# Optimization experiments

Hardware: AMD Instinct MI355X
Metric: run time of the kernel (lower is better)

The kernel has to match this reference:

```python
import jax, jax.numpy as jnp
import numpy as np
import math

NUM_HEADS = 16
HIDDEN = 1024
HEAD_DIM = HIDDEN // NUM_HEADS
MAX_POS = 512
BUCKET = 256
SCALE = 1.0 / math.sqrt(3.0 * HEAD_DIM)


def _make_log_bucket_position(rel_pos):
    # rel_pos: int32 [S, S]
    mid = BUCKET // 2
    rp = rel_pos.astype(jnp.float32)
    sign = jnp.sign(rp)
    abs_pos = jnp.where((rel_pos < mid) & (rel_pos > -mid), float(mid - 1), jnp.abs(rp))
    log_pos = jnp.ceil(jnp.log(abs_pos / mid) * (mid - 1) / math.log((MAX_POS - 1) / mid)) + mid
    bucket_pos = jnp.where(abs_pos <= mid, rp, log_pos * sign)
    return bucket_pos.astype(jnp.int32)


def _get_rel_pos(num_positions):
    ids = jnp.arange(num_positions, dtype=jnp.int32)
    rel_pos = ids[:, None] - ids[None, :]  # [S, S]
    return _make_log_bucket_position(rel_pos)


def setup_inputs() -> dict:
    key = jax.random.key(0)
    ks = jax.random.split(key, 10)
    B, S = 8, 512
    s_in = 1.0 / math.sqrt(HIDDEN)
    inputs = jax.random.normal(ks[0], (B, S, HIDDEN), dtype=jnp.float32)
    rel_embeddings = jax.random.normal(ks[1], (B, 2 * BUCKET, HIDDEN), dtype=jnp.float32)
    Wq = jax.random.normal(ks[2], (HIDDEN, NUM_HEADS, HEAD_DIM), dtype=jnp.float32) * s_in
    Wk = jax.random.normal(ks[3], (HIDDEN, NUM_HEADS, HEAD_DIM), dtype=jnp.float32) * s_in
    Wv = jax.random.normal(ks[4], (HIDDEN, NUM_HEADS, HEAD_DIM), dtype=jnp.float32) * s_in
    bq = jnp.zeros((NUM_HEADS, HEAD_DIM), dtype=jnp.float32)
    bk = jnp.zeros((NUM_HEADS, HEAD_DIM), dtype=jnp.float32)
    bv = jnp.zeros((NUM_HEADS, HEAD_DIM), dtype=jnp.float32)
    Wo = jax.random.normal(ks[5], (HIDDEN, HIDDEN), dtype=jnp.float32) * s_in
    bo = jnp.zeros((HIDDEN,), dtype=jnp.float32)
    return {"inputs": inputs, "rel_embeddings": rel_embeddings,
            "Wq": Wq, "bq": bq, "Wk": Wk, "bk": bk, "Wv": Wv, "bv": bv,
            "Wo": Wo, "bo": bo}


def reference(inputs, rel_embeddings, Wq, bq, Wk, bk, Wv, bv, Wo, bo):
    B, S, _ = inputs.shape
    # projections: [B,S,H,D]
    query = jnp.einsum('bsc,chd->bshd', inputs, Wq) + bq
    key = jnp.einsum('bsc,chd->bshd', inputs, Wk) + bk
    value = jnp.einsum('bsc,chd->bshd', inputs, Wv) + bv

    # content-content scores: [B,H,S_q,S_k]
    scores = jnp.einsum('bkhd,bqhd->bhqk', key, query) * SCALE

    # relative position projections on rel_embeddings [B,P,hidden], P=2*BUCKET
    pos_query = jnp.einsum('bpc,chd->bphd', rel_embeddings, Wq) + bq
    pos_key = jnp.einsum('bpc,chd->bphd', rel_embeddings, Wk) + bk

    rel_pos = _get_rel_pos(S)  # [S,S] int32
    span = BUCKET

    # c2p: query vs pos_key -> [B,H,S,P], gather along last axis
    c2p = jnp.einsum('bphd,bqhd->bhqp', pos_key, query)
    c2p_pos = jnp.clip(rel_pos + span, 0, 2 * span - 1)  # [S,S]
    c2p_idx = jnp.broadcast_to(c2p_pos[None, None], (B, NUM_HEADS, S, S))
    c2p = jnp.take_along_axis(c2p, c2p_idx, axis=3) * SCALE

    # p2c: key vs pos_query -> [B,H,S,P], gather then transpose
    p2c = jnp.einsum('bphd,bkhd->bhkp', pos_query, key)
    p2c_pos = jnp.clip(-rel_pos + span, 0, 2 * span - 1)
    p2c_idx = jnp.broadcast_to(p2c_pos[None, None], (B, NUM_HEADS, S, S))
    p2c = jnp.take_along_axis(p2c, p2c_idx, axis=3)
    p2c = jnp.swapaxes(p2c, 2, 3) * SCALE

    scores = scores + c2p + p2c
    probs = jax.nn.softmax(scores.astype(jnp.float32), axis=-1).astype(inputs.dtype)

    # attend: [B,S,H,D] -> [B,S,hidden]
    attn_out = jnp.einsum('bhqk,bkhd->bqhd', probs, value)
    attn_out = attn_out.reshape(B, S, HIDDEN)
    return jnp.einsum('bsc,cd->bsd', attn_out, Wo) + bo
```

## Files before the change

### kernel.cpp

```cpp
#include <hip/hip_runtime.h>

#define NUM_HEADS 16
#define HEAD_DIM  64
#define HIDDEN    1024
#define SEQ       512
#define BATCH     8
#define NBH       128
#define POSN      512
#define SCALE_F   0.07216878364870323f

typedef __attribute__((ext_vector_type(8))) short  short8;
typedef __attribute__((ext_vector_type(4))) short  short4_t;
typedef __attribute__((ext_vector_type(4))) float  floatx4;

#define GLDS16(gsrc, ldst) \
    __builtin_amdgcn_global_load_lds((const __attribute__((address_space(1))) void*)(gsrc), \
                                     (__attribute__((address_space(3))) void*)(ldst), 16, 0, 0)

__device__ __forceinline__ float bits2f(short s) {
    union { unsigned u; float f; } x;
    x.u = ((unsigned)(unsigned short)s) << 16;
    return x.f;
}
__device__ __forceinline__ short f2bits(float f) {
    union { float f; unsigned u; } x;
    x.f = f;
    unsigned r = x.u + 0x7fffu + ((x.u >> 16) & 1u);
    return (short)(r >> 16);
}

__global__ void conv_pair(const float* __restrict__ a, const float* __restrict__ b,
                          short* __restrict__ oa, short* __restrict__ ob)
{
    const int idx = blockIdx.x * 256 + threadIdx.x;
    floatx4 va = ((const floatx4*)a)[idx];
    floatx4 vb = ((const floatx4*)b)[idx];
    short4_t ra, rb;
#pragma unroll
    for (int i = 0; i < 4; i++) { ra[i] = f2bits(va[i]); rb[i] = f2bits(vb[i]); }
    ((short4_t*)oa)[idx] = ra;
    ((short4_t*)ob)[idx] = rb;
}

__global__ void wtrans(const float* __restrict__ w0, const float* __restrict__ w1,
                       const float* __restrict__ w2, const float* __restrict__ w3,
                       short* __restrict__ o0, short* __restrict__ o1,
                       short* __restrict__ o2, short* __restrict__ o3)
{
    __shared__ float tile[64][65];
    const int z = blockIdx.z;
    const float* src = (z == 0) ? w0 : (z == 1) ? w1 : (z == 2) ? w2 : w3;
    short*       dst = (z == 0) ? o0 : (z == 1) ? o1 : (z == 2) ? o2 : o3;
    const int c0 = blockIdx.x * 64, n0 = blockIdx.y * 64;
    const int t = threadIdx.x;
#pragma unroll
    for (int j = 0; j < 16; j++) {
        const int e = t + j * 256;
        tile[e >> 6][e & 63] = src[(long)(c0 + (e >> 6)) * 1024 + n0 + (e & 63)];
    }
    __syncthreads();
#pragma unroll
    for (int j = 0; j < 16; j++) {
        const int e = t + j * 256;
        dst[(long)(n0 + (e >> 6)) * 1024 + c0 + (e & 63)] = f2bits(tile[e & 63][e >> 6]);
    }
}

__global__ void ftab_build(int* __restrict__ ftab)
{
    const int i = blockIdx.x * 256 + threadIdx.x;
    if (i >= 1023) return;
    const int delta = i - 511;
    const float Cf = (float)log(511.0 / 128.0);
    float absp = (delta < 128 && delta > -128) ? 127.0f : fabsf((float)delta);
    float bucket;
    if (absp <= 128.0f) {
        bucket = (float)delta;
    } else {
        float lp = ceilf((logf(absp * (1.0f / 128.0f)) * 127.0f) / Cf) + 128.0f;
        bucket = (delta > 0) ? lp : -lp;
    }
    int bi = (int)bucket + 256;
    bi = min(max(bi, 0), 511);
    ftab[i] = bi;
}

template<int MODE>
__global__ __launch_bounds__(256)
void gemm_nt(const short* __restrict__ A, long aBatch, int lda,
             const short* __restrict__ BT, long bBatch, int ldb,
             void* __restrict__ O0, void* __restrict__ O1, void* __restrict__ O2,
             long oBatch, int ldo,
             const float* __restrict__ b0, const float* __restrict__ b1,
             const float* __restrict__ b2, int Kd,
             const short* __restrict__ A2,
             void* __restrict__ O3, void* __restrict__ O4)
{
    __shared__ __align__(16) short As[2][128 * 64];
    __shared__ __align__(16) short Bs[2][128 * 64];

    int m0, n0, yy = 0;
    bool z1 = false;
    const int z = blockIdx.z;
    if (MODE == 6) {
        const int lin = blockIdx.x + (blockIdx.y << 5);
        const int swz = (lin & 7) * 160 + (lin >> 3);
        m0 = (swz & 31) * 128;
        yy = swz >> 5;
        z1 = (yy >= 24);
        n0 = (z1 ? (yy - 24) : yy) * 128;
    } else {
        m0 = blockIdx.x * 128;
        n0 = blockIdx.y * 128;
    }

    const short* Ab;
    const short* Bb;
    if (MODE == 6) {
        Ab = z1 ? A2 : A;
        Bb = BT;
    } else {
        Ab = A + (long)z * aBatch;
        Bb = BT + (long)z * bBatch;
    }

    const int t = threadIdx.x;
    const int l = t & 63, w = t >> 6;
    const int wm = w >> 1, wn = w & 1;
    const int lr = l & 15, lg = l >> 4;

    floatx4 acc[4][4];
#pragma unroll
    for (int i = 0; i < 4; i++)
#pragma unroll
        for (int j = 0; j < 4; j++) acc[i][j] = (floatx4){0.f, 0.f, 0.f, 0.f};

#pragma unroll
    for (int j = 0; j < 4; j++) {
        const int c = (w * 4 + j) * 64 + l;
        const int row = c >> 3, pc = c & 7;
        const int cc = pc ^ (row & 7);
        GLDS16(Ab + (long)(m0 + row) * lda + cc * 8, As[0] + c * 8);
        GLDS16(Bb + (long)(n0 + row) * ldb + cc * 8, Bs[0] + c * 8);
    }
    __syncthreads();

    int cur = 0;
    for (int k0 = 0; k0 < Kd; k0 += 64, cur ^= 1) {
        if (k0 + 64 < Kd) {
            const int kn = k0 + 64;
#pragma unroll
            for (int j = 0; j < 4; j++) {
                const int c = (w * 4 + j) * 64 + l;
                const int row = c >> 3, pc = c & 7;
                const int cc = pc ^ (row & 7);
                GLDS16(Ab + (long)(m0 + row) * lda + kn + cc * 8, As[cur ^ 1] + c * 8);
                GLDS16(Bb + (long)(n0 + row) * ldb + kn + cc * 8, Bs[cur ^ 1] + c * 8);
            }
        }
#pragma unroll
        for (int ks = 0; ks < 2; ks++) {
            short8 af[4], bfr[4];
#pragma unroll
            for (int i = 0; i < 4; i++) {
                const int mr = wm * 64 + i * 16 + lr;
                af[i] = *(const short8*)((char*)As[cur] + mr * 128 + (((ks * 4 + lg) ^ (mr & 7)) * 16));
                const int nr = wn * 64 + i * 16 + lr;
                bfr[i] = *(const short8*)((char*)Bs[cur] + nr * 128 + (((ks * 4 + lg) ^ (nr & 7)) * 16));
            }
#pragma unroll
            for (int i = 0; i < 4; i++)
#pragma unroll
                for (int j = 0; j < 4; j++)
                    acc[i][j] = __builtin_amdgcn_mfma_f32_16x16x32_bf16(af[i], bfr[j], acc[i][j], 0, 0, 0);
        }
        __syncthreads();
    }

    if (MODE == 6 && !z1 && yy >= 16) {
        short* tp = &As[0][0];
#pragma unroll
        for (int i = 0; i < 4; i++)
#pragma unroll
            for (int j = 0; j < 4; j++)
#pragma unroll
                for (int e = 0; e < 4; e++) {
                    const int ml  = wm * 64 + i * 16 + lg * 4 + e;
                    const int ngl = wn * 64 + j * 16 + lr;
                    const float v = acc[i][j][e] + b2[(n0 & 1023) + ngl];
                    tp[ngl * 128 + (ml ^ ((ngl & 7) << 4))] = f2bits(v);
                }
        __syncthreads();
        const int b = m0 >> 9, s0 = m0 & 511;
        const int hb = (n0 & 1023) >> 6;
        short* dst = (short*)O2;
#pragma unroll
        for (int j = 0; j < 8; j++) {
            const int task = t + j * 256;
            const int r = task >> 4, c = task & 15;
            short8 v8 = *(const short8*)(tp + r * 128 + ((c * 8) ^ ((r & 7) << 4)));
            const int h = hb + (r >> 6), d = r & 63;
            *(short8*)(dst + ((long)((b * NUM_HEADS + h) * HEAD_DIM + d)) * SEQ + s0 + c * 8) = v8;
        }
        return;
    }

#pragma unroll
    for (int i = 0; i < 4; i++) {
#pragma unroll
        for (int j = 0; j < 4; j++) {
#pragma unroll
            for (int e = 0; e < 4; e++) {
                const int mg = m0 + wm * 64 + i * 16 + lg * 4 + e;
                const int ng = n0 + wn * 64 + j * 16 + lr;
                float v = acc[i][j][e];
                if (MODE == 1) {
                    ((short*)O0)[(long)z * oBatch + (long)mg * ldo + ng] = f2bits(v);
                } else if (MODE == 2) {
                    ((float*)O0)[(long)mg * ldo + ng] = v + b0[ng];
                } else if (MODE == 6) {
                    const int hh = ng & 1023, mat = ng >> 10;
                    const int h = hh >> 6, d = hh & 63;
                    const int b = mg >> 9, s = mg & 511;
                    v += (mat == 0 ? b0 : b1)[hh];
                    short* dst;
                    if (z1) dst = (short*)(mat == 0 ? O3 : O4);
                    else    dst = (short*)(mat == 0 ? O0 : O1);
                    dst[((long)(b * NUM_HEADS + h) * SEQ + s) * HEAD_DIM + d] = f2bits(v);
                }
            }
        }
    }
}

__global__ __launch_bounds__(512, 2)
void p2c_fused(const short* __restrict__ posQ, const short* __restrict__ K,
               const int* __restrict__ ftab, short* __restrict__ G)
{
    __shared__ __align__(16) short As[512 * 64];
    __shared__ __align__(16) short Bs[64 * 64];
    __shared__ short ft[1024];
    const int ko = blockIdx.x, bh = blockIdx.y;
    const int k0 = ko * 64;
    const int t = threadIdx.x, l = t & 63, w = t >> 6;
    const int lr = l & 15, lg = l >> 4;
    const short* Ab = posQ + (long)bh * SEQ * HEAD_DIM;
    const short* Kb = K + (long)bh * SEQ * HEAD_DIM;

    for (int i = t; i < 1024; i += 512) ft[i] = (short)((i < 1023) ? ftab[i] : 0);

#pragma unroll
    for (int j = 0; j < 8; j++) {
        const int c = j * 512 + t;
        const int row = c >> 3, pc = c & 7;
        const int cc = pc ^ (row & 7);
        GLDS16(Ab + (long)row * HEAD_DIM + cc * 8, As + c * 8);
    }
    {
        const int c = t;
        const int row = c >> 3, pc = c & 7;
        const int cc = pc ^ (row & 7);
        GLDS16(Kb + (long)(k0 + row) * HEAD_DIM + cc * 8, Bs + c * 8);
    }
    __syncthreads();

    floatx4 acc[4][4];
#pragma unroll
    for (int i = 0; i < 4; i++)
#pragma unroll
        for (int j = 0; j < 4; j++) acc[i][j] = (floatx4){0.f, 0.f, 0.f, 0.f};
#pragma unroll
    for (int ks = 0; ks < 2; ks++) {
        short8 af[4], bfr[4];
#pragma unroll
        for (int i = 0; i < 4; i++) {
            const int mr = w * 64 + i * 16 + lr;
            af[i] = *(const short8*)((char*)As + mr * 128 + (((ks * 4 + lg) ^ (mr & 7)) * 16));
            const int nr = i * 16 + lr;
            bfr[i] = *(const short8*)((char*)Bs + nr * 128 + (((ks * 4 + lg) ^ (nr & 7)) * 16));
        }
#pragma unroll
        for (int i = 0; i < 4; i++)
#pragma unroll
            for (int j = 0; j < 4; j++)
                acc[i][j] = __builtin_amdgcn_mfma_f32_16x16x32_bf16(af[i], bfr[j], acc[i][j], 0, 0, 0);
    }
    __syncthreads();

#pragma unroll
    for (int i = 0; i < 4; i++)
#pragma unroll
        for (int j = 0; j < 4; j++)
#pragma unroll
            for (int e = 0; e < 4; e++) {
                const int p = w * 64 + i * 16 + lg * 4 + e;
                const int kk = j * 16 + lr;
                As[p * 64 + (kk ^ (lg << 4))] = f2bits(acc[i][j][e]);
            }
    __syncthreads();

    short* Gb = G + (long)bh * SEQ * SEQ;
#pragma unroll
    for (int j = 0; j < 8; j++) {
        const int task = j * 512 + t;
        const int q = task >> 3, kc = task & 7;
        short8 v;
#pragma unroll
        for (int i = 0; i < 8; i++) {
            const int kl = kc * 8 + i;
            const int fk = (int)ft[q - (k0 + kl) + 511];
            v[i] = As[fk * 64 + (kl ^ (((fk >> 2) & 3) << 4))];
        }
        *(short8*)(Gb + (long)q * SEQ + k0 + kc * 8) = v;
    }
}

__global__ __launch_bounds__(256, 4)
void attn_fused(const short* __restrict__ Q, const short* __restrict__ K,
                const short* __restrict__ Vt,
                const short* __restrict__ c2pf, const short* __restrict__ Gp2c,
                const int* __restrict__ ftab,
                short* __restrict__ attnO)
{
    __shared__ __align__(16) short c2pS[32 * 512];
    __shared__ float red[2][4][32];
    __shared__ short ft[1024];

    const int lin  = blockIdx.x;
    const int lin2 = (lin & 7) * 256 + (lin >> 3);
    const int bh = lin2 >> 4, qt = lin2 & 15;
    const int q0 = qt * 32;
    const int t = threadIdx.x, l = t & 63, w = t >> 6;
    const int lr = l & 15, lg = l >> 4;
    const long pbase = (long)bh * SEQ * HEAD_DIM;
    const short* Qb  = Q  + pbase;
    const short* Kb  = K  + pbase;
    const short* Vtb = Vt + pbase;
    const short* c2pb = c2pf + (long)bh * SEQ * POSN;
    const short* Gb   = Gp2c + (long)bh * SEQ * SEQ;

    for (int i = t; i < 1024; i += 256) ft[i] = (short)((i < 1023) ? ftab[i] : 0);

#pragma unroll
    for (int j = 0; j < 8; j++) {
        const int c = w * 512 + j * 64 + l;
        const int row = c >> 6, cc = c & 63;
        GLDS16(c2pb + (long)(q0 + row) * POSN + (cc ^ (row & 7)) * 8, c2pS + c * 8);
    }

    short8 aq[2][2];
#pragma unroll
    for (int mt = 0; mt < 2; mt++)
#pragma unroll
        for (int ks = 0; ks < 2; ks++)
            aq[mt][ks] = *(const short8*)(Qb + (q0 + mt * 16 + lr) * 64 + ks * 32 + lg * 8);

    floatx4 acc[2][8];
#pragma unroll
    for (int mt = 0; mt < 2; mt++)
#pragma unroll
        for (int nt = 0; nt < 8; nt++) acc[mt][nt] = (floatx4){0.f, 0.f, 0.f, 0.f};

#pragma unroll
    for (int nt = 0; nt < 8; nt++) {
        const int kr = w * 128 + nt * 16 + lr;
        short8 kb0 = *(const short8*)(Kb + kr * 64 + lg * 8);
        short8 kb1 = *(const short8*)(Kb + kr * 64 + 32 + lg * 8);
#pragma unroll
        for (int mt = 0; mt < 2; mt++) {
            acc[mt][nt] = __builtin_amdgcn_mfma_f32_16x16x32_bf16(aq[mt][0], kb0, acc[mt][nt], 0, 0, 0);
            acc[mt][nt] = __builtin_amdgcn_mfma_f32_16x16x32_bf16(aq[mt][1], kb1, acc[mt][nt], 0, 0, 0);
        }
    }

    __syncthreads();

#pragma unroll
    for (int mt = 0; mt < 2; mt++)
#pragma unroll
        for (int nt = 0; nt < 8; nt++) {
            const int k = w * 128 + nt * 16 + lr;
#pragma unroll
            for (int e = 0; e < 4; e++) {
                const int r = mt * 16 + lg * 4 + e;
                const int fk = (int)ft[q0 + r - k + 511];
                acc[mt][nt][e] = (acc[mt][nt][e]
                                  + bits2f(c2pS[r * 512 + (fk ^ ((r & 7) << 3))])
                                  + bits2f(Gb[(long)(q0 + r) * SEQ + k])) * SCALE_F;
            }
        }

#pragma unroll
    for (int mt = 0; mt < 2; mt++)
#pragma unroll
        for (int e = 0; e < 4; e++) {
            float m = acc[mt][0][e];
#pragma unroll
            for (int nt = 1; nt < 8; nt++) m = fmaxf(m, acc[mt][nt][e]);
            m = fmaxf(m, __shfl_xor(m, 1));
            m = fmaxf(m, __shfl_xor(m, 2));
            m = fmaxf(m, __shfl_xor(m, 4));
            m = fmaxf(m, __shfl_xor(m, 8));
            red[0][w][mt * 16 + lg * 4 + e] = m;
        }
    __syncthreads();

#pragma unroll
    for (int mt = 0; mt < 2; mt++)
#pragma unroll
        for (int e = 0; e < 4; e++) {
            const int r = mt * 16 + lg * 4 + e;
            const float m = fmaxf(fmaxf(red[0][0][r], red[0][1][r]),
                                  fmaxf(red[0][2][r], red[0][3][r]));
            float s = 0.f;
#pragma unroll
            for (int nt = 0; nt < 8; nt++) {
                float p = __expf(acc[mt][nt][e] - m);
                acc[mt][nt][e] = p;
                s += p;
            }
            s += __shfl_xor(s, 1); s += __shfl_xor(s, 2);
            s += __shfl_xor(s, 4); s += __shfl_xor(s, 8);
            red[1][w][r] = s;
#pragma unroll
            for (int nt = 0; nt < 8; nt++) {
                const int kcol = w * 128 + nt * 16 + lr;
                int byte = r * 1024 + kcol * 2;
                byte ^= (r & 7) << 4;
                *(short*)((char*)c2pS + byte) = f2bits(acc[mt][nt][e]);
            }
        }
    __syncthreads();

    floatx4 accO[2];
    accO[0] = (floatx4){0.f, 0.f, 0.f, 0.f};
    accO[1] = (floatx4){0.f, 0.f, 0.f, 0.f};
#pragma unroll
    for (int ks = 0; ks < 16; ks++) {
        short8 vb = *(const short8*)(Vtb + (long)(w * 16 + lr) * SEQ + ks * 32 + lg * 8);
#pragma unroll
        for (int mt = 0; mt < 2; mt++) {
            const int qr = mt * 16 + lr;
            int byte = qr * 1024 + (ks * 32 + lg * 8) * 2;
            byte ^= (qr & 7) << 4;
            short8 pa = *(const short8*)((char*)c2pS + byte);
            accO[mt] = __builtin_amdgcn_mfma_f32_16x16x32_bf16(pa, vb, accO[mt], 0, 0, 0);
        }
    }

    const int b = bh >> 4, h = bh & 15;
#pragma unroll
    for (int mt = 0; mt < 2; mt++)
#pragma unroll
        for (int e = 0; e < 4; e++) {
            const int r = mt * 16 + lg * 4 + e;
            const float rs = red[1][0][r] + red[1][1][r] + red[1][2][r] + red[1][3][r];
            const float v = accO[mt][e] / rs;
            attnO[((long)(b * SEQ + q0 + r)) * HIDDEN + h * HEAD_DIM + w * 16 + lr] = f2bits(v);
        }
}

extern "C" void kernel_launch(void* const* d_in, const int* in_sizes, int n_in,
                              void* d_out, int out_size, void* d_ws, size_t ws_size,
                              hipStream_t stream)
{
    const float* inputs = (const float*)d_in[0];
    const float* rel    = (const float*)d_in[1];
    const float* Wq     = (const float*)d_in[2];
    const float* bq     = (const float*)d_in[3];
    const float* Wk     = (const float*)d_in[4];
    const float* bk     = (const float*)d_in[5];
    const float* Wv     = (const float*)d_in[6];
    const float* bv     = (const float*)d_in[7];
    const float* Wo     = (const float*)d_in[8];
    const float* bo     = (const float*)d_in[9];
    float* out = (float*)d_out;

    char* ws = (char*)d_ws;
    size_t off = 0;
    auto alloc = [&](size_t bytes) -> char* {
        char* p = ws + off;
        off += (bytes + 255) & ~(size_t)255;
        return p;
    };
    short* inA   = (short*)alloc(4194304ull * 2);
    short* inRel = (short*)alloc(4194304ull * 2);
    short* WqT   = (short*)alloc(1048576ull * 2);
    short* WkT   = (short*)alloc(1048576ull * 2);
    short* WvT   = (short*)alloc(1048576ull * 2);
    short* WoT   = (short*)alloc(1048576ull * 2);
    short* Qw    = (short*)alloc(4194304ull * 2);
    short* Kw    = (short*)alloc(4194304ull * 2);
    short* Vtw   = (short*)alloc(4194304ull * 2);
    short* posQw = (short*)alloc(4194304ull * 2);
    short* posKw = (short*)alloc(4194304ull * 2);
    short* c2pW  = (short*)alloc(33554432ull * 2);
    short* GW    = (short*)alloc(33554432ull * 2);
    short* attnW = (short*)alloc(4194304ull * 2);
    int*   ftabW = (int*)alloc(4096);

    conv_pair<<<4096, 256, 0, stream>>>(inputs, rel, inA, inRel);
    wtrans<<<dim3(16, 16, 4), 256, 0, stream>>>(Wq, Wk, Wv, Wo, WqT, WkT, WvT, WoT);
    ftab_build<<<4, 256, 0, stream>>>(ftabW);

    gemm_nt<6><<<dim3(32, 40), 256, 0, stream>>>(inA, 0, 1024, WqT, 0, 1024,
                                                 Qw, Kw, Vtw, 0, 0, bq, bk, bv, 1024,
                                                 inRel, posQw, posKw);

    gemm_nt<1><<<dim3(4, 4, 128), 256, 0, stream>>>(Qw, 32768, 64, posKw, 32768, 64,
                                                    c2pW, nullptr, nullptr, 262144, 512,
                                                    nullptr, nullptr, nullptr, 64,
                                                    nullptr, nullptr, nullptr);

    p2c_fused<<<dim3(8, 128), 512, 0, stream>>>(posQw, Kw, ftabW, GW);

    attn_fused<<<2048, 256, 0, stream>>>(Qw, Kw, Vtw, c2pW, GW, ftabW, attnW);

    gemm_nt<2><<<dim3(32, 8), 256, 0, stream>>>(attnW, 0, 1024, WoT, 0, 1024,
                                                out, nullptr, nullptr, 0, 1024, bo, nullptr, nullptr, 1024,
                                                nullptr, nullptr, nullptr);
}
```

Baseline: 204.6 us.

## Fold c2p gather into p2c kernel and write fragment-ordered bias tensor

The p2c kernel now also gathers the c2p value for each (q,k) and writes the summed bias to a new tensor laid out in 32-row query tiles with k-major, fragment-friendly order. The attention kernel then loads this bias directly into registers matching its MFMA accumulator layout. This removes its LDS staging of c2p rows, the index-table gather and the scattered G reads. The cost is an uncoalesced gather of c2p from global memory inside p2c, plus bf16 rounding of the summed bias.

```diff
diff --git a/kernel.cpp b/kernel.cpp
--- a/kernel.cpp
+++ b/kernel.cpp
@@ -235,7 +235,8 @@
 
 __global__ __launch_bounds__(512, 2)
 void p2c_fused(const short* __restrict__ posQ, const short* __restrict__ K,
-               const int* __restrict__ ftab, short* __restrict__ G)
+               const short* __restrict__ c2pf, const int* __restrict__ ftab,
+               short* __restrict__ Bias)
 {
     __shared__ __align__(16) short As[512 * 64];
     __shared__ __align__(16) short Bs[64 * 64];
@@ -246,6 +247,7 @@
     const int lr = l & 15, lg = l >> 4;
     const short* Ab = posQ + (long)bh * SEQ * HEAD_DIM;
     const short* Kb = K + (long)bh * SEQ * HEAD_DIM;
+    const short* c2pb = c2pf + (long)bh * SEQ * POSN;
 
     for (int i = t; i < 1024; i += 512) ft[i] = (short)((i < 1023) ? ftab[i] : 0);
 
@@ -299,32 +301,34 @@
             }
     __syncthreads();
 
-    short* Gb = G + (long)bh * SEQ * SEQ;
+    short* Bb = Bias + (long)bh * SEQ * SEQ;
 #pragma unroll
     for (int j = 0; j < 8; j++) {
         const int task = j * 512 + t;
-        const int q = task >> 3, kc = task & 7;
+        const int qt = task >> 8;
+        const int kl = (task >> 2) & 63;
+        const int rc = task & 3;
+        const int k  = k0 + kl;
         short8 v;
 #pragma unroll
         for (int i = 0; i < 8; i++) {
-            const int kl = kc * 8 + i;
-            const int fk = (int)ft[q - (k0 + kl) + 511];
-            v[i] = As[fk * 64 + (kl ^ (((fk >> 2) & 3) << 4))];
-        }
-        *(short8*)(Gb + (long)q * SEQ + k0 + kc * 8) = v;
+            const int q  = qt * 32 + rc * 8 + i;
+            const int fk = (int)ft[q - k + 511];
+            const float sv = bits2f(As[fk * 64 + (kl ^ (((fk >> 2) & 3) << 4))]);
+            const float cv = bits2f(c2pb[(long)q * POSN + fk]);
+            v[i] = f2bits(sv + cv);
+        }
+        *(short8*)(Bb + (((long)qt * 512 + k) << 5) + rc * 8) = v;
     }
 }
 
 __global__ __launch_bounds__(256, 4)
 void attn_fused(const short* __restrict__ Q, const short* __restrict__ K,
-                const short* __restrict__ Vt,
-                const short* __restrict__ c2pf, const short* __restrict__ Gp2c,
-                const int* __restrict__ ftab,
+                const short* __restrict__ Vt, const short* __restrict__ Bias,
                 short* __restrict__ attnO)
 {
-    __shared__ __align__(16) short c2pS[32 * 512];
+    __shared__ __align__(16) short PS[32 * 512];
     __shared__ float red[2][4][32];
-    __shared__ short ft[1024];
 
     const int lin  = blockIdx.x;
     const int lin2 = (lin & 7) * 256 + (lin >> 3);
@@ -336,17 +340,16 @@
     const short* Qb  = Q  + pbase;
     const short* Kb  = K  + pbase;
     const short* Vtb = Vt + pbase;
-    const short* c2pb = c2pf + (long)bh * SEQ * POSN;
-    const short* Gb   = Gp2c + (long)bh * SEQ * SEQ;
-
-    for (int i = t; i < 1024; i += 256) ft[i] = (short)((i < 1023) ? ftab[i] : 0);
-
-#pragma unroll
-    for (int j = 0; j < 8; j++) {
-        const int c = w * 512 + j * 64 + l;
-        const int row = c >> 6, cc = c & 63;
-        GLDS16(c2pb + (long)(q0 + row) * POSN + (cc ^ (row & 7)) * 8, c2pS + c * 8);
-    }
+    const short* Bb  = Bias + ((long)bh * 16 + qt) * (512 * 32);
+
+    short4_t bfrag[2][8];
+#pragma unroll
+    for (int mt = 0; mt < 2; mt++)
+#pragma unroll
+        for (int nt = 0; nt < 8; nt++) {
+            const int k = w * 128 + nt * 16 + lr;
+            bfrag[mt][nt] = *(const short4_t*)(Bb + (long)k * 32 + mt * 16 + lg * 4);
+        }
 
     short8 aq[2][2];
 #pragma unroll
@@ -373,22 +376,13 @@
         }
     }
 
-    __syncthreads();
-
-#pragma unroll
-    for (int mt = 0; mt < 2; mt++)
-#pragma unroll
-        for (int nt = 0; nt < 8; nt++) {
-            const int k = w * 128 + nt * 16 + lr;
-#pragma unroll
-            for (int e = 0; e < 4; e++) {
-                const int r = mt * 16 + lg * 4 + e;
-                const int fk = (int)ft[q0 + r - k + 511];
-                acc[mt][nt][e] = (acc[mt][nt][e]
-                                  + bits2f(c2pS[r * 512 + (fk ^ ((r & 7) << 3))])
-                                  + bits2f(Gb[(long)(q0 + r) * SEQ + k])) * SCALE_F;
-            }
-        }
+#pragma unroll
+    for (int mt = 0; mt < 2; mt++)
+#pragma unroll
+        for (int nt = 0; nt < 8; nt++)
+#pragma unroll
+            for (int e = 0; e < 4; e++)
+                acc[mt][nt][e] = (acc[mt][nt][e] + bits2f(bfrag[mt][nt][e])) * SCALE_F;
 
 #pragma unroll
     for (int mt = 0; mt < 2; mt++)
@@ -427,7 +421,7 @@
                 const int kcol = w * 128 + nt * 16 + lr;
                 int byte = r * 1024 + kcol * 2;
                 byte ^= (r & 7) << 4;
-                *(short*)((char*)c2pS + byte) = f2bits(acc[mt][nt][e]);
+                *(short*)((char*)PS + byte) = f2bits(acc[mt][nt][e]);
             }
         }
     __syncthreads();
@@ -443,7 +437,7 @@
             const int qr = mt * 16 + lr;
             int byte = qr * 1024 + (ks * 32 + lg * 8) * 2;
             byte ^= (qr & 7) << 4;
-            short8 pa = *(const short8*)((char*)c2pS + byte);
+            short8 pa = *(const short8*)((char*)PS + byte);
             accO[mt] = __builtin_amdgcn_mfma_f32_16x16x32_bf16(pa, vb, accO[mt], 0, 0, 0);
         }
     }
@@ -495,7 +489,7 @@
     short* posQw = (short*)alloc(4194304ull * 2);
     short* posKw = (short*)alloc(4194304ull * 2);
     short* c2pW  = (short*)alloc(33554432ull * 2);
-    short* GW    = (short*)alloc(33554432ull * 2);
+    short* BW    = (short*)alloc(33554432ull * 2);
     short* attnW = (short*)alloc(4194304ull * 2);
     int*   ftabW = (int*)alloc(4096);
 
@@ -512,9 +506,9 @@
                                                     nullptr, nullptr, nullptr, 64,
                                                     nullptr, nullptr, nullptr);
 
-    p2c_fused<<<dim3(8, 128), 512, 0, stream>>>(posQw, Kw, ftabW, GW);
-
-    attn_fused<<<2048, 256, 0, stream>>>(Qw, Kw, Vtw, c2pW, GW, ftabW, attnW);
+    p2c_fused<<<dim3(8, 128), 512, 0, stream>>>(posQw, Kw, c2pW, ftabW, BW);
+
+    attn_fused<<<2048, 256, 0, stream>>>(Qw, Kw, Vtw, BW, attnW);
 
     gemm_nt<2><<<dim3(32, 8), 256, 0, stream>>>(attnW, 0, 1024, WoT, 0, 1024,
                                                 out, nullptr, nullptr, 0, 1024, bo, nullptr, nullptr, 1024,
```

Result: no change. 207.5 us (+1.4%).
